# Performance work log

Measured on AMD Instinct MI355X. Metric: run time of the kernel, lower is better.

The kernel has to match this reference:

```python
import jax, jax.numpy as jnp
import numpy as np

B, N, T, FM = 2, 768, 96, 8
HID = 64
TD = HID // 2   # temporal_dim = max(8, 32) = 32
MD = HID // 2   # mark_hidden_dim = 32


def _lin_init(key, fan_in, fan_out):
    k1, k2 = jax.random.split(key)
    bound = 1.0 / np.sqrt(fan_in)
    w = jax.random.uniform(k1, (fan_in, fan_out), minval=-bound, maxval=bound, dtype=jnp.float32)
    b = jax.random.uniform(k2, (fan_out,), minval=-bound, maxval=bound, dtype=jnp.float32)
    return w, b


def setup_inputs() -> dict:
    key = jax.random.key(0)
    ks = jax.random.split(key, 16)
    x_hist = jax.random.normal(ks[0], (B, N, T), dtype=jnp.float32)
    x_mark = jax.random.normal(ks[1], (B, N, T, FM), dtype=jnp.float32)
    a_static = jax.random.uniform(ks[2], (N, N), dtype=jnp.float32)
    te_w1, te_b1 = _lin_init(ks[3], 3, TD)
    te_w2, te_b2 = _lin_init(ks[4], TD, TD)
    me_w1, me_b1 = _lin_init(ks[5], FM, MD)
    me_w2, me_b2 = _lin_init(ks[6], MD, MD)
    nf_w, nf_b = _lin_init(ks[7], TD + MD, HID)
    ps_w1, ps_b1 = _lin_init(ks[8], 3 * HID, HID)
    ps_w2, ps_b2 = _lin_init(ks[9], HID, 1)
    raw_lambda = jnp.array([np.log(0.1 / 0.9)], dtype=jnp.float32)  # logit(lambda_init)
    return dict(x_hist=x_hist, x_mark=x_mark, a_static=a_static,
                te_w1=te_w1, te_b1=te_b1, te_w2=te_w2, te_b2=te_b2,
                me_w1=me_w1, me_b1=me_b1, me_w2=me_w2, me_b2=me_b2,
                nf_w=nf_w, nf_b=nf_b,
                ps_w1=ps_w1, ps_b1=ps_b1, ps_w2=ps_w2, ps_b2=ps_b2,
                raw_lambda=raw_lambda)


def reference(x_hist, x_mark, a_static,
              te_w1, te_b1, te_w2, te_b2,
              me_w1, me_b1, me_w2, me_b2,
              nf_w, nf_b, ps_w1, ps_b1, ps_w2, ps_b2, raw_lambda):
    n = x_hist.shape[1]
    # temporal stats: last / mean / max over T -> [B,N,3]
    stats = jnp.stack([x_hist[:, :, -1], x_hist.mean(axis=-1), x_hist.max(axis=-1)], axis=-1)
    h_t = jax.nn.relu(stats @ te_w1 + te_b1) @ te_w2 + te_b2          # [B,N,TD]
    mark_sum = x_mark.mean(axis=2)                                    # [B,N,FM]
    h_m = jax.nn.relu(mark_sum @ me_w1 + me_b1) @ me_w2 + me_b2       # [B,N,MD]
    h = jax.nn.relu(jnp.concatenate([h_t, h_m], axis=-1) @ nf_w + nf_b)  # [B,N,H]
    # pair scorer: Linear([h_i, h_j, |h_i-h_j|]) decomposed over the 3 blocks
    hdim = h.shape[-1]
    w_i, w_j, w_d = ps_w1[:hdim], ps_w1[hdim:2 * hdim], ps_w1[2 * hdim:]
    s_i = h @ w_i                                                     # [B,N,H]
    s_j = h @ w_j                                                     # [B,N,H]
    diff = jnp.abs(h[:, :, None, :] - h[:, None, :, :])               # [B,N,N,H]
    pre = s_i[:, :, None, :] + s_j[:, None, :, :] + diff @ w_d + ps_b1
    delta = jnp.tanh((jax.nn.relu(pre) @ ps_w2 + ps_b2)[..., 0])      # [B,N,N]
    eye = jnp.eye(n, dtype=delta.dtype)
    delta = delta * (1.0 - eye)
    delta = 0.5 * (delta + jnp.swapaxes(delta, 1, 2))                 # sym_graph
    lam = jax.nn.sigmoid(raw_lambda)                                  # [1]
    a_hybrid = a_static[None] + lam * delta
    a_hybrid = jax.nn.relu(a_hybrid)                                  # nonneg_mode='relu'
    d = jnp.clip(a_hybrid.sum(axis=-1, keepdims=True), 1e-6, None)    # row norm
    a_hybrid = a_hybrid / d
    return a_hybrid, lam
```

## Files before the change

### kernel.cpp

```cpp
#include <hip/hip_runtime.h>
#include <hip/hip_bf16.h>
#include <math.h>

#define B_ 2
#define N_ 768
#define T_ 96
#define FM_ 8
#define HID_ 64
#define TD_ 32
#define MD_ 32
#define TILE 16
#define TI32 32
#define NTILES (N_/TILE)
#define PERB 600
#define SSTR 68

typedef __attribute__((ext_vector_type(8))) short short8v;
typedef __attribute__((ext_vector_type(4))) float f32x4;
typedef __attribute__((ext_vector_type(4))) unsigned int uint4v;

__device__ __forceinline__ unsigned int pack_bf2(float d0, float d1){
  __hip_bfloat162 t = __float22bfloat162_rn(make_float2(d0, d1));
  unsigned int u;
  __builtin_memcpy(&u, &t, 4);
  return u;
}

__device__ __forceinline__ float ftanh(float x){
  float e = __expf(2.f * x);
  return 1.f - 2.f * __builtin_amdgcn_rcpf(e + 1.f);
}

__device__ __forceinline__ float wave_sum64(float v){
  #pragma unroll
  for (int m = 32; m; m >>= 1) v += __shfl_xor(v, m);
  return v;
}
__device__ __forceinline__ float wave_max64(float v){
  #pragma unroll
  for (int m = 32; m; m >>= 1) v = fmaxf(v, __shfl_xor(v, m));
  return v;
}

__global__ __launch_bounds__(64) void feat_kernel(
    const float* __restrict__ x_hist, const float* __restrict__ x_mark,
    const float* __restrict__ te_w1, const float* __restrict__ te_b1,
    const float* __restrict__ te_w2, const float* __restrict__ te_b2,
    const float* __restrict__ me_w1, const float* __restrict__ me_b1,
    const float* __restrict__ me_w2, const float* __restrict__ me_b2,
    const float* __restrict__ nf_w,  const float* __restrict__ nf_b,
    const float* __restrict__ ps_w1,
    float* __restrict__ h_out, float* __restrict__ si_out, float* __restrict__ sj_out,
    unsigned short* __restrict__ wdf)
{
  const int lane = threadIdx.x;

  if (blockIdx.x >= B_ * N_) {
    const int q  = blockIdx.x - B_ * N_;
    const int nt = q >> 1, s = q & 1;
    const int col = (lane & 15) + 16 * nt;
    const int k0  = s * 32 + ((lane >> 4) << 3);
    #pragma unroll
    for (int jj = 0; jj < 8; ++jj) {
      float v = ps_w1[(2 * HID_ + k0 + jj) * HID_ + col];
      __hip_bfloat16 bv = __float2bfloat16(v);
      unsigned short us;
      __builtin_memcpy(&us, &bv, 2);
      wdf[(q * 64 + lane) * 8 + jj] = us;
    }
    return;
  }

  const int row = blockIdx.x;

  __shared__ float st[3];
  __shared__ float ms[FM_];
  __shared__ float t1s[TD_];
  __shared__ float m1s[MD_];
  __shared__ float hc[HID_];
  __shared__ float hs[HID_];

  const float* xh = x_hist + (long)row * T_;
  float s  = xh[lane];
  float mx = s;
  if (lane < T_ - 64) { float v = xh[lane + 64]; s += v; mx = fmaxf(mx, v); }
  s  = wave_sum64(s);
  mx = wave_max64(mx);
  if (lane == 0) { st[0] = xh[T_ - 1]; st[1] = s * (1.0f / T_); st[2] = mx; }

  const float* xm = x_mark + (long)row * T_ * FM_;
  float msv = 0.f;
  #pragma unroll
  for (int k = 0; k < 12; ++k) msv += xm[lane + 64 * k];
  msv += __shfl_xor(msv, 8);
  msv += __shfl_xor(msv, 16);
  msv += __shfl_xor(msv, 32);
  if (lane < FM_) ms[lane] = msv * (1.0f / T_);
  __syncthreads();

  if (lane < TD_) {
    float a = te_b1[lane];
    #pragma unroll
    for (int k = 0; k < 3; ++k) a += st[k] * te_w1[k * TD_ + lane];
    t1s[lane] = fmaxf(a, 0.f);
    float am = me_b1[lane];
    #pragma unroll
    for (int k = 0; k < FM_; ++k) am += ms[k] * me_w1[k * MD_ + lane];
    m1s[lane] = fmaxf(am, 0.f);
  }
  __syncthreads();
  if (lane < TD_) {
    float a = te_b2[lane];
    #pragma unroll
    for (int k = 0; k < TD_; ++k) a += t1s[k] * te_w2[k * TD_ + lane];
    hc[lane] = a;
    float am = me_b2[lane];
    #pragma unroll
    for (int k = 0; k < MD_; ++k) am += m1s[k] * me_w2[k * MD_ + lane];
    hc[TD_ + lane] = am;
  }
  __syncthreads();
  {
    float a = nf_b[lane];
    #pragma unroll
    for (int k = 0; k < HID_; ++k) a += hc[k] * nf_w[k * HID_ + lane];
    float hv = fmaxf(a, 0.f);
    hs[lane] = hv;
    h_out[(long)row * HID_ + lane] = hv;
  }
  __syncthreads();
  {
    float a1 = 0.f, a2 = 0.f;
    #pragma unroll
    for (int k = 0; k < HID_; ++k) {
      float hv = hs[k];
      a1 += hv * ps_w1[k * HID_ + lane];
      a2 += hv * ps_w1[(HID_ + k) * HID_ + lane];
    }
    si_out[(long)row * HID_ + lane] = a1;
    sj_out[(long)row * HID_ + lane] = a2;
  }
}

__global__ __launch_bounds__(256, 3) void pair_kernel(
    const float* __restrict__ h, const float* __restrict__ si, const float* __restrict__ sj,
    const float* __restrict__ ps_b1, const float* __restrict__ ps_w2,
    const float* __restrict__ ps_b2, const unsigned short* __restrict__ wdf,
    float* __restrict__ delta)
{
  int bidx = blockIdx.x;
  int b = bidx / PERB;
  int t = bidx % PERB;
  int a = 0;
  while (t >= NTILES - 2 * a) { t -= NTILES - 2 * a; ++a; }
  int tJ = 2 * a + t;
  const int i0 = a * TI32, j0 = tJ * TILE;

  __shared__ float hI  [TI32][HID_];
  __shared__ float hJT [HID_][TILE + 1];
  __shared__ float SIIb[TI32][SSTR];
  __shared__ float SJI_[TI32][SSTR];
  __shared__ float SIJb[TILE][SSTR];
  __shared__ float SJJ_[TILE][SSTR];
  __shared__ float w2s [HID_];

  const int tid  = threadIdx.x;
  const int lane = tid & 63;
  const int w    = tid >> 6;

  {
    const int r  = tid >> 4;
    const int c4 = (tid & 15) * 4;
    const f32x4 b14 = *(const f32x4*)(ps_b1 + c4);
    #pragma unroll
    for (int p = 0; p < 2; ++p) {
      const int rr = r + p * 16;
      const long gi = ((long)b * N_ + i0 + rr) * HID_ + c4;
      *(f32x4*)&hI  [rr][c4] = *(const f32x4*)(h  + gi);
      *(f32x4*)&SIIb[rr][c4] = *(const f32x4*)(si + gi) + b14;
      *(f32x4*)&SJI_[rr][c4] = *(const f32x4*)(sj + gi);
    }
    const long gj = ((long)b * N_ + j0 + r) * HID_ + c4;
    f32x4 vhj = *(const f32x4*)(h + gj);
    #pragma unroll
    for (int q = 0; q < 4; ++q) hJT[c4 + q][r] = vhj[q];
    *(f32x4*)&SIJb[r][c4] = *(const f32x4*)(si + gj) + b14;
    *(f32x4*)&SJJ_[r][c4] = *(const f32x4*)(sj + gj);
    if (tid < 16) *(f32x4*)&w2s[tid * 4] = *(const f32x4*)(ps_w2 + tid * 4);
  }
  const float b2 = ps_b2[0];
  __syncthreads();

  const int g   = lane >> 4;
  const int c16 = lane & 15;

  short8v wfr[8];
  const short8v* wdp = (const short8v*)wdf;
  #pragma unroll
  for (int q = 0; q < 8; ++q) wfr[q] = wdp[q * 64 + lane];

  float hJv[2][8];
  #pragma unroll
  for (int s = 0; s < 2; ++s)
    #pragma unroll
    for (int jj = 0; jj < 8; ++jj)
      hJv[s][jj] = hJT[32 * s + 8 * g + jj][c16];

  f32x4 sJJ4h[4], sIJ4h[4], w24h[4];
  #pragma unroll
  for (int mt = 0; mt < 4; ++mt) {
    const int cb = 16 * mt + 4 * g;
    sJJ4h[mt] = *(const f32x4*)&SJJ_[c16][cb];
    sIJ4h[mt] = *(const f32x4*)&SIJb[c16][cb];
    w24h[mt]  = *(const f32x4*)&w2s[cb];
  }

  float* drow = delta + (long)b * N_ * N_;

  #pragma unroll
  for (int m = 0; m < 8; ++m) {
    const int iloc = w * 8 + m;
    const int i = i0 + iloc;

    short8v afr[2];
    #pragma unroll
    for (int s = 0; s < 2; ++s) {
      f32x4 ha = *(const f32x4*)&hI[iloc][32 * s + 8 * g];
      f32x4 hb = *(const f32x4*)&hI[iloc][32 * s + 8 * g + 4];
      uint4v uv;
      #pragma unroll
      for (int p = 0; p < 2; ++p) {
        float d0 = fabsf(ha[2*p]   - hJv[s][2*p]);
        float d1 = fabsf(ha[2*p+1] - hJv[s][2*p+1]);
        uv[p] = pack_bf2(d0, d1);
      }
      #pragma unroll
      for (int p = 0; p < 2; ++p) {
        float d0 = fabsf(hb[2*p]   - hJv[s][4 + 2*p]);
        float d1 = fabsf(hb[2*p+1] - hJv[s][4 + 2*p+1]);
        uv[2 + p] = pack_bf2(d0, d1);
      }
      afr[s] = __builtin_bit_cast(short8v, uv);
    }

    f32x4 acc[4];
    #pragma unroll
    for (int mt = 0; mt < 4; ++mt) acc[mt] = (f32x4){0.f, 0.f, 0.f, 0.f};
    #pragma unroll
    for (int s = 0; s < 2; ++s)
      #pragma unroll
      for (int mt = 0; mt < 4; ++mt)
        acc[mt] = __builtin_amdgcn_mfma_f32_16x16x32_bf16(wfr[2 * mt + s], afr[s], acc[mt], 0, 0, 0);

    float a1 = 0.f, a2 = 0.f;
    #pragma unroll
    for (int mt = 0; mt < 4; ++mt) {
      const int cb = 16 * mt + 4 * g;
      f32x4 sII4 = *(const f32x4*)&SIIb[iloc][cb];
      f32x4 sJI4 = *(const f32x4*)&SJI_[iloc][cb];
      #pragma unroll
      for (int r = 0; r < 4; ++r) {
        float av = acc[mt][r];
        a1 += fmaxf(av + sII4[r] + sJJ4h[mt][r], 0.f) * w24h[mt][r];
        a2 += fmaxf(av + sJI4[r] + sIJ4h[mt][r], 0.f) * w24h[mt][r];
      }
    }
    a1 += __shfl_xor(a1, 16);  a1 += __shfl_xor(a1, 32);
    a2 += __shfl_xor(a2, 16);  a2 += __shfl_xor(a2, 32);

    if (g == 0) {
      const int j = j0 + c16;
      if (i < j) {
        float sym = 0.5f * (ftanh(a1 + b2) + ftanh(a2 + b2));
        drow[(long)i * N_ + j] = sym;
        drow[(long)j * N_ + i] = sym;
      } else if (i == j) {
        drow[(long)i * N_ + i] = 0.f;
      }
    }
  }
}

__global__ __launch_bounds__(256) void norm_kernel(
    const float* __restrict__ a_static, const float* __restrict__ raw_lambda,
    float* __restrict__ out)
{
  const int row = blockIdx.x;
  const int i   = row % N_;
  const int tid = threadIdx.x;
  const float lam = 1.f / (1.f + expf(-raw_lambda[0]));

  const float* arow = a_static + (long)i * N_;
  float* drow = out + (long)row * N_;

  float vals[3];
  float s = 0.f;
  #pragma unroll
  for (int r = 0; r < 3; ++r) {
    int j = r * 256 + tid;
    float v = arow[j] + lam * drow[j];
    v = fmaxf(v, 0.f);
    vals[r] = v;
    s += v;
  }
  s = wave_sum64(s);
  __shared__ float ps[4];
  if ((tid & 63) == 0) ps[tid >> 6] = s;
  __syncthreads();
  float tot = ps[0] + ps[1] + ps[2] + ps[3];
  float inv = 1.f / fmaxf(tot, 1e-6f);
  #pragma unroll
  for (int r = 0; r < 3; ++r) {
    int j = r * 256 + tid;
    drow[j] = vals[r] * inv;
  }
  if (row == 0 && tid == 0) out[(long)B_ * N_ * N_] = lam;
}

extern "C" void kernel_launch(void* const* d_in, const int* in_sizes, int n_in,
                              void* d_out, int out_size, void* d_ws, size_t ws_size,
                              hipStream_t stream) {
  const float* x_hist     = (const float*)d_in[0];
  const float* x_mark     = (const float*)d_in[1];
  const float* a_static   = (const float*)d_in[2];
  const float* te_w1      = (const float*)d_in[3];
  const float* te_b1      = (const float*)d_in[4];
  const float* te_w2      = (const float*)d_in[5];
  const float* te_b2      = (const float*)d_in[6];
  const float* me_w1      = (const float*)d_in[7];
  const float* me_b1      = (const float*)d_in[8];
  const float* me_w2      = (const float*)d_in[9];
  const float* me_b2      = (const float*)d_in[10];
  const float* nf_w       = (const float*)d_in[11];
  const float* nf_b       = (const float*)d_in[12];
  const float* ps_w1      = (const float*)d_in[13];
  const float* ps_b1      = (const float*)d_in[14];
  const float* ps_w2      = (const float*)d_in[15];
  const float* ps_b2      = (const float*)d_in[16];
  const float* raw_lambda = (const float*)d_in[17];

  float* out = (float*)d_out;
  float* h   = (float*)d_ws;
  float* si  = h  + (long)B_ * N_ * HID_;
  float* sj  = si + (long)B_ * N_ * HID_;
  unsigned short* wdf = (unsigned short*)(sj + (long)B_ * N_ * HID_);

  feat_kernel<<<B_ * N_ + 8, 64, 0, stream>>>(
      x_hist, x_mark, te_w1, te_b1, te_w2, te_b2,
      me_w1, me_b1, me_w2, me_b2, nf_w, nf_b, ps_w1, h, si, sj, wdf);

  pair_kernel<<<B_ * PERB, 256, 0, stream>>>(
      h, si, sj, ps_b1, ps_w2, ps_b2, wdf, out);

  norm_kernel<<<B_ * N_, 256, 0, stream>>>(a_static, raw_lambda, out);
}
```

Baseline: 35.60 us.

## Interleave pair-scorer bias tiles for packed float2 math and batch feat rows per block

```diff
diff --git a/kernel.cpp b/kernel.cpp
--- a/kernel.cpp
+++ b/kernel.cpp
@@ -13,10 +13,11 @@
 #define TI32 32
 #define NTILES (N_/TILE)
 #define PERB 600
-#define SSTR 68
+#define SJSTR 66
 
 typedef __attribute__((ext_vector_type(8))) short short8v;
 typedef __attribute__((ext_vector_type(4))) float f32x4;
+typedef __attribute__((ext_vector_type(2))) float f32x2;
 typedef __attribute__((ext_vector_type(4))) unsigned int uint4v;
 
 __device__ __forceinline__ unsigned int pack_bf2(float d0, float d1){
@@ -42,7 +43,7 @@
   return v;
 }
 
-__global__ __launch_bounds__(64) void feat_kernel(
+__global__ __launch_bounds__(256) void feat_kernel(
     const float* __restrict__ x_hist, const float* __restrict__ x_mark,
     const float* __restrict__ te_w1, const float* __restrict__ te_b1,
     const float* __restrict__ te_w2, const float* __restrict__ te_b2,
@@ -53,10 +54,13 @@
     float* __restrict__ h_out, float* __restrict__ si_out, float* __restrict__ sj_out,
     unsigned short* __restrict__ wdf)
 {
-  const int lane = threadIdx.x;
-
-  if (blockIdx.x >= B_ * N_) {
-    const int q  = blockIdx.x - B_ * N_;
+  const int tid  = threadIdx.x;
+  const int lane = tid & 63;
+  const int w    = tid >> 6;
+  const int NB   = (B_ * N_) / 4;
+
+  if (blockIdx.x >= NB) {
+    const int q  = (blockIdx.x - NB) * 4 + w;
     const int nt = q >> 1, s = q & 1;
     const int col = (lane & 15) + 16 * nt;
     const int k0  = s * 32 + ((lane >> 4) << 3);
@@ -71,14 +75,14 @@
     return;
   }
 
-  const int row = blockIdx.x;
-
-  __shared__ float st[3];
-  __shared__ float ms[FM_];
-  __shared__ float t1s[TD_];
-  __shared__ float m1s[MD_];
-  __shared__ float hc[HID_];
-  __shared__ float hs[HID_];
+  const int row = blockIdx.x * 4 + w;
+
+  __shared__ float st [4][3];
+  __shared__ float ms [4][FM_];
+  __shared__ float t1s[4][TD_];
+  __shared__ float m1s[4][MD_];
+  __shared__ float hc [4][HID_];
+  __shared__ float hs [4][HID_];
 
   const float* xh = x_hist + (long)row * T_;
   float s  = xh[lane];
@@ -86,7 +90,7 @@
   if (lane < T_ - 64) { float v = xh[lane + 64]; s += v; mx = fmaxf(mx, v); }
   s  = wave_sum64(s);
   mx = wave_max64(mx);
-  if (lane == 0) { st[0] = xh[T_ - 1]; st[1] = s * (1.0f / T_); st[2] = mx; }
+  if (lane == 0) { st[w][0] = xh[T_ - 1]; st[w][1] = s * (1.0f / T_); st[w][2] = mx; }
 
   const float* xm = x_mark + (long)row * T_ * FM_;
   float msv = 0.f;
@@ -95,37 +99,37 @@
   msv += __shfl_xor(msv, 8);
   msv += __shfl_xor(msv, 16);
   msv += __shfl_xor(msv, 32);
-  if (lane < FM_) ms[lane] = msv * (1.0f / T_);
+  if (lane < FM_) ms[w][lane] = msv * (1.0f / T_);
   __syncthreads();
 
   if (lane < TD_) {
     float a = te_b1[lane];
     #pragma unroll
-    for (int k = 0; k < 3; ++k) a += st[k] * te_w1[k * TD_ + lane];
-    t1s[lane] = fmaxf(a, 0.f);
+    for (int k = 0; k < 3; ++k) a += st[w][k] * te_w1[k * TD_ + lane];
+    t1s[w][lane] = fmaxf(a, 0.f);
     float am = me_b1[lane];
     #pragma unroll
-    for (int k = 0; k < FM_; ++k) am += ms[k] * me_w1[k * MD_ + lane];
-    m1s[lane] = fmaxf(am, 0.f);
+    for (int k = 0; k < FM_; ++k) am += ms[w][k] * me_w1[k * MD_ + lane];
+    m1s[w][lane] = fmaxf(am, 0.f);
   }
   __syncthreads();
   if (lane < TD_) {
     float a = te_b2[lane];
     #pragma unroll
-    for (int k = 0; k < TD_; ++k) a += t1s[k] * te_w2[k * TD_ + lane];
-    hc[lane] = a;
+    for (int k = 0; k < TD_; ++k) a += t1s[w][k] * te_w2[k * TD_ + lane];
+    hc[w][lane] = a;
     float am = me_b2[lane];
     #pragma unroll
-    for (int k = 0; k < MD_; ++k) am += m1s[k] * me_w2[k * MD_ + lane];
-    hc[TD_ + lane] = am;
+    for (int k = 0; k < MD_; ++k) am += m1s[w][k] * me_w2[k * MD_ + lane];
+    hc[w][TD_ + lane] = am;
   }
   __syncthreads();
   {
     float a = nf_b[lane];
     #pragma unroll
-    for (int k = 0; k < HID_; ++k) a += hc[k] * nf_w[k * HID_ + lane];
+    for (int k = 0; k < HID_; ++k) a += hc[w][k] * nf_w[k * HID_ + lane];
     float hv = fmaxf(a, 0.f);
-    hs[lane] = hv;
+    hs[w][lane] = hv;
     h_out[(long)row * HID_ + lane] = hv;
   }
   __syncthreads();
@@ -133,7 +137,7 @@
     float a1 = 0.f, a2 = 0.f;
     #pragma unroll
     for (int k = 0; k < HID_; ++k) {
-      float hv = hs[k];
+      float hv = hs[w][k];
       a1 += hv * ps_w1[k * HID_ + lane];
       a2 += hv * ps_w1[(HID_ + k) * HID_ + lane];
     }
@@ -158,11 +162,8 @@
 
   __shared__ float hI  [TI32][HID_];
   __shared__ float hJT [HID_][TILE + 1];
-  __shared__ float SIIb[TI32][SSTR];
-  __shared__ float SJI_[TI32][SSTR];
-  __shared__ float SIJb[TILE][SSTR];
-  __shared__ float SJJ_[TILE][SSTR];
-  __shared__ float w2s [HID_];
+  __shared__ f32x2 SI2 [TI32][HID_];
+  __shared__ f32x2 SJ2 [TILE][SJSTR];
 
   const int tid  = threadIdx.x;
   const int lane = tid & 63;
@@ -176,17 +177,20 @@
     for (int p = 0; p < 2; ++p) {
       const int rr = r + p * 16;
       const long gi = ((long)b * N_ + i0 + rr) * HID_ + c4;
-      *(f32x4*)&hI  [rr][c4] = *(const f32x4*)(h  + gi);
-      *(f32x4*)&SIIb[rr][c4] = *(const f32x4*)(si + gi) + b14;
-      *(f32x4*)&SJI_[rr][c4] = *(const f32x4*)(sj + gi);
+      *(f32x4*)&hI[rr][c4] = *(const f32x4*)(h + gi);
+      f32x4 vii = *(const f32x4*)(si + gi) + b14;
+      f32x4 vji = *(const f32x4*)(sj + gi);
+      #pragma unroll
+      for (int q = 0; q < 4; ++q) SI2[rr][c4 + q] = (f32x2){vii[q], vji[q]};
     }
     const long gj = ((long)b * N_ + j0 + r) * HID_ + c4;
     f32x4 vhj = *(const f32x4*)(h + gj);
     #pragma unroll
     for (int q = 0; q < 4; ++q) hJT[c4 + q][r] = vhj[q];
-    *(f32x4*)&SIJb[r][c4] = *(const f32x4*)(si + gj) + b14;
-    *(f32x4*)&SJJ_[r][c4] = *(const f32x4*)(sj + gj);
-    if (tid < 16) *(f32x4*)&w2s[tid * 4] = *(const f32x4*)(ps_w2 + tid * 4);
+    f32x4 vij = *(const f32x4*)(si + gj) + b14;
+    f32x4 vjj = *(const f32x4*)(sj + gj);
+    #pragma unroll
+    for (int q = 0; q < 4; ++q) SJ2[r][c4 + q] = (f32x2){vjj[q], vij[q]};
   }
   const float b2 = ps_b2[0];
   __syncthreads();
@@ -206,13 +210,19 @@
     for (int jj = 0; jj < 8; ++jj)
       hJv[s][jj] = hJT[32 * s + 8 * g + jj][c16];
 
-  f32x4 sJJ4h[4], sIJ4h[4], w24h[4];
+  f32x2 sJ2h[16];
+  float w2h[16];
   #pragma unroll
   for (int mt = 0; mt < 4; ++mt) {
     const int cb = 16 * mt + 4 * g;
-    sJJ4h[mt] = *(const f32x4*)&SJJ_[c16][cb];
-    sIJ4h[mt] = *(const f32x4*)&SIJb[c16][cb];
-    w24h[mt]  = *(const f32x4*)&w2s[cb];
+    f32x4 u0 = *(const f32x4*)&SJ2[c16][cb];
+    f32x4 u1 = *(const f32x4*)&SJ2[c16][cb + 2];
+    sJ2h[mt*4+0] = (f32x2){u0[0], u0[1]};
+    sJ2h[mt*4+1] = (f32x2){u0[2], u0[3]};
+    sJ2h[mt*4+2] = (f32x2){u1[0], u1[1]};
+    sJ2h[mt*4+3] = (f32x2){u1[2], u1[3]};
+    #pragma unroll
+    for (int r = 0; r < 4; ++r) w2h[mt*4+r] = ps_w2[cb + r];
   }
 
   float* drow = delta + (long)b * N_ * N_;
@@ -252,19 +262,24 @@
       for (int mt = 0; mt < 4; ++mt)
         acc[mt] = __builtin_amdgcn_mfma_f32_16x16x32_bf16(wfr[2 * mt + s], afr[s], acc[mt], 0, 0, 0);
 
-    float a1 = 0.f, a2 = 0.f;
+    f32x2 acc2 = (f32x2){0.f, 0.f};
     #pragma unroll
     for (int mt = 0; mt < 4; ++mt) {
       const int cb = 16 * mt + 4 * g;
-      f32x4 sII4 = *(const f32x4*)&SIIb[iloc][cb];
-      f32x4 sJI4 = *(const f32x4*)&SJI_[iloc][cb];
+      f32x4 s01 = *(const f32x4*)&SI2[iloc][cb];
+      f32x4 s23 = *(const f32x4*)&SI2[iloc][cb + 2];
       #pragma unroll
       for (int r = 0; r < 4; ++r) {
+        f32x2 siv = (r < 2) ? (f32x2){s01[2*r], s01[2*r+1]}
+                            : (f32x2){s23[2*(r-2)], s23[2*(r-2)+1]};
         float av = acc[mt][r];
-        a1 += fmaxf(av + sII4[r] + sJJ4h[mt][r], 0.f) * w24h[mt][r];
-        a2 += fmaxf(av + sJI4[r] + sIJ4h[mt][r], 0.f) * w24h[mt][r];
+        f32x2 pre = siv + sJ2h[mt*4+r];
+        pre = pre + (f32x2){av, av};
+        pre = __builtin_elementwise_max(pre, (f32x2){0.f, 0.f});
+        acc2 = acc2 + pre * (f32x2){w2h[mt*4+r], w2h[mt*4+r]};
       }
     }
+    float a1 = acc2[0], a2 = acc2[1];
     a1 += __shfl_xor(a1, 16);  a1 += __shfl_xor(a1, 32);
     a2 += __shfl_xor(a2, 16);  a2 += __shfl_xor(a2, 32);
 
@@ -345,7 +360,7 @@
   float* sj  = si + (long)B_ * N_ * HID_;
   unsigned short* wdf = (unsigned short*)(sj + (long)B_ * N_ * HID_);
 
-  feat_kernel<<<B_ * N_ + 8, 64, 0, stream>>>(
+  feat_kernel<<<(B_ * N_) / 4 + 2, 256, 0, stream>>>(
       x_hist, x_mark, te_w1, te_b1, te_w2, te_b2,
       me_w1, me_b1, me_w2, me_b2, nf_w, nf_b, ps_w1, h, si, sj, wdf);
 
```

After: 36.62 us. +2.9%, slower.
